# Performance work log

Hardware: AMD Instinct MI355X
Metric: run time of the kernel (lower is better)

The kernel has to match this reference:

```python
import jax, jax.numpy as jnp
import numpy as np

DIM_B = 4096   # batch of ragged segments
DIM_M = 128    # max seq len == dim_m == dim_c (source: dim_c = dim_m)
DIM_C = 128
DIM_Q = 256    # dim_q = 2 * dim_m


def _make_lengths():
    # deterministic ragged lengths in [1, DIM_M]; 37 coprime with 128 -> exact total
    return ((np.arange(DIM_B) * 37) % DIM_M + 1).astype(np.int64)


def setup_inputs() -> dict:
    key = jax.random.key(0)
    k1, k2, k3, k4 = jax.random.split(key, 4)
    xss = jax.random.normal(k1, (DIM_B, DIM_M, DIM_Q), dtype=jnp.float32)
    Wk = jax.random.normal(k2, (DIM_C, DIM_Q), dtype=jnp.float32) * 0.05
    Wc = jax.random.normal(k3, (DIM_M, DIM_C), dtype=jnp.float32) * 0.05
    proj = jax.random.normal(k4, (DIM_C, DIM_Q), dtype=jnp.float32) * 0.05
    lens = _make_lengths()
    # flat padded index (b*DIM_M + s) of every valid ragged token, in batch order
    gather_idx = np.concatenate([b * DIM_M + np.arange(l) for b, l in enumerate(lens)]).astype(np.int64)
    return {
        "xss": xss,
        "Wk": Wk,
        "Wc": Wc,
        "proj": proj,
        "seq_lengths": jnp.asarray(lens),
        "gather_idx": jnp.asarray(gather_idx),
    }


def reference(xss, Wk, Wc, proj, seq_lengths, gather_idx):
    B, M, Q = xss.shape
    # validity mask over padded positions
    mask = (jnp.arange(M)[None, :] < seq_lengths[:, None]).astype(xss.dtype)  # (B, M)
    # kernel: Linear(dim_q -> dim_c), applied to all (padded) tokens
    ks = jnp.einsum('bmq,cq->bmc', xss, Wk)          # (B, M, C)
    # pool: masked sum over the ragged segment
    context = jnp.einsum('bmc,bm->bc', ks, mask)     # (B, C)
    cs = context @ Wc.T                              # (B, C)  (dim_m == dim_c)
    v = cs @ proj                                    # (B, Q)
    y = jnp.einsum('bq,bmq->bm', v, xss)             # (B, M) per-token scalar
    # gather valid ragged tokens in original concat order -> (total_tokens, 1)
    ys = y.reshape(-1)[gather_idx][:, None]
    return ys
```

## Files before the change

kernel.cpp:

```cpp
#include <hip/hip_runtime.h>
#include <hip/hip_bf16.h>

#define DIM_B 4096
#define DIM_M 128
#define DIM_C 128
#define DIM_Q 256

__global__ __launch_bounds__(256) void k_xsum(const float* __restrict__ xss,
                                              const int* __restrict__ lens32,
                                              float* __restrict__ xsum) {
    const int b = blockIdx.x;
    const int tid = threadIdx.x;
    const int wave = tid >> 6, lane = tid & 63;
    const bool is64 = (lens32[1] == 0);
    const int len = is64 ? lens32[2 * b] : lens32[b];
    const float* base = xss + (size_t)b * DIM_M * DIM_Q + lane * 4;
    float a0 = 0.f, a1 = 0.f, a2 = 0.f, a3 = 0.f;
    for (int m = wave; m < len; m += 4) {
        const float4 u = *(const float4*)(base + (size_t)m * DIM_Q);
        a0 += u.x; a1 += u.y; a2 += u.z; a3 += u.w;
    }
    __shared__ float s[4][DIM_Q];
    s[wave][lane * 4 + 0] = a0;
    s[wave][lane * 4 + 1] = a1;
    s[wave][lane * 4 + 2] = a2;
    s[wave][lane * 4 + 3] = a3;
    __syncthreads();
    xsum[(size_t)b * DIM_Q + tid] = s[0][tid] + s[1][tid] + s[2][tid] + s[3][tid];
}

__global__ __launch_bounds__(256) void k_a1(const float* __restrict__ Wc,
                                            const float* __restrict__ proj,
                                            float* __restrict__ A1) {
    const int c = blockIdx.x;
    const int qp = threadIdx.x;
    float acc = 0.f;
    for (int j = 0; j < DIM_M; ++j)
        acc += Wc[j * DIM_C + c] * proj[j * DIM_Q + qp];
    A1[c * DIM_Q + qp] = acc;
}

__global__ __launch_bounds__(256) void k_wcomb(const float* __restrict__ Wk,
                                               const float* __restrict__ A1,
                                               float* __restrict__ Wcomb) {
    const int q = blockIdx.x;
    const int qp = threadIdx.x;
    float acc = 0.f;
    for (int c = 0; c < DIM_C; ++c)
        acc += Wk[c * DIM_Q + q] * A1[c * DIM_Q + qp];
    Wcomb[q * DIM_Q + qp] = acc;
}

__global__ __launch_bounds__(256) void k_v(const float* __restrict__ xsum,
                                           const float* __restrict__ Wcomb,
                                           float* __restrict__ v) {
    const int tid = threadIdx.x;
    const int b0 = blockIdx.x * 16;
    __shared__ float s[16][DIM_Q];
    for (int r = 0; r < 16; ++r)
        s[r][tid] = xsum[(size_t)(b0 + r) * DIM_Q + tid];
    __syncthreads();
    float acc[16];
#pragma unroll
    for (int r = 0; r < 16; ++r) acc[r] = 0.f;
    for (int q = 0; q < DIM_Q; ++q) {
        const float w = Wcomb[q * DIM_Q + tid];
#pragma unroll
        for (int r = 0; r < 16; ++r) acc[r] += s[r][q] * w;
    }
#pragma unroll
    for (int r = 0; r < 16; ++r)
        v[(size_t)(b0 + r) * DIM_Q + tid] = acc[r];
}

__global__ __launch_bounds__(256) void k_y(const float* __restrict__ xss,
                                           const float* __restrict__ v,
                                           const int* __restrict__ gidx32,
                                           float* __restrict__ out,
                                           int ntok) {
    const int wave = threadIdx.x >> 6, lane = threadIdx.x & 63;
    const int t = blockIdx.x * 4 + wave;
    if (t >= ntok) return;
    const bool is64 = (gidx32[1] == 0);
    const int idx = is64 ? gidx32[2 * t] : gidx32[t];
    const int b = idx >> 7;
    const float4 u  = *(const float4*)(xss + (size_t)idx * DIM_Q + lane * 4);
    const float4 vv = *(const float4*)(v + (size_t)b * DIM_Q + lane * 4);
    float d = u.x * vv.x + u.y * vv.y + u.z * vv.z + u.w * vv.w;
#pragma unroll
    for (int off = 32; off >= 1; off >>= 1)
        d += __shfl_down(d, off, 64);
    if (lane == 0)
        out[t] = d;
}

extern "C" void kernel_launch(void* const* d_in, const int* in_sizes, int n_in,
                              void* d_out, int out_size, void* d_ws, size_t ws_size,
                              hipStream_t stream) {
    const float* xss  = (const float*)d_in[0];
    const float* Wk   = (const float*)d_in[1];
    const float* Wc   = (const float*)d_in[2];
    const float* proj = (const float*)d_in[3];
    const int* lens = (const int*)d_in[4];
    const int* gidx = (const int*)d_in[5];
    float* out = (float*)d_out;
    const int ntok = in_sizes[5];

    float* ws    = (float*)d_ws;
    float* xsum  = ws;
    float* vbuf  = ws + (size_t)DIM_B * DIM_Q;
    float* A1    = vbuf + (size_t)DIM_B * DIM_Q;
    float* Wcomb = A1 + (size_t)DIM_C * DIM_Q;

    k_xsum<<<DIM_B, 256, 0, stream>>>(xss, lens, xsum);
    k_a1<<<DIM_C, 256, 0, stream>>>(Wc, proj, A1);
    k_wcomb<<<DIM_Q, 256, 0, stream>>>(Wk, A1, Wcomb);
    k_v<<<DIM_B / 16, 256, 0, stream>>>(xsum, Wcomb, vbuf);
    k_y<<<(ntok + 3) / 4, 256, 0, stream>>>(xss, vbuf, gidx, out, ntok);
}
```

Before: 744.4 us.

## Fuse pooling, projection and per-token dot into one kernel with LDS row staging

Replaces the xsum, v and y kernels with one per-batch kernel that sums the valid rows, computes v from Wcomb, and then computes per-token dot products. The first 56 rows are staged in shared memory so the second pass mostly avoids re-reading xss from HBM. Output offsets come from an in-block prefix sum of lengths instead of gather_idx. This trades heavy LDS use (lower occupancy) and redundant per-block Wcomb matvec and prefix-sum work for roughly halving global traffic.

```diff
diff --git a/kernel.cpp b/kernel.cpp
--- a/kernel.cpp
+++ b/kernel.cpp
@@ -1,33 +1,10 @@
 #include <hip/hip_runtime.h>
-#include <hip/hip_bf16.h>
 
 #define DIM_B 4096
 #define DIM_M 128
 #define DIM_C 128
 #define DIM_Q 256
-
-__global__ __launch_bounds__(256) void k_xsum(const float* __restrict__ xss,
-                                              const int* __restrict__ lens32,
-                                              float* __restrict__ xsum) {
-    const int b = blockIdx.x;
-    const int tid = threadIdx.x;
-    const int wave = tid >> 6, lane = tid & 63;
-    const bool is64 = (lens32[1] == 0);
-    const int len = is64 ? lens32[2 * b] : lens32[b];
-    const float* base = xss + (size_t)b * DIM_M * DIM_Q + lane * 4;
-    float a0 = 0.f, a1 = 0.f, a2 = 0.f, a3 = 0.f;
-    for (int m = wave; m < len; m += 4) {
-        const float4 u = *(const float4*)(base + (size_t)m * DIM_Q);
-        a0 += u.x; a1 += u.y; a2 += u.z; a3 += u.w;
-    }
-    __shared__ float s[4][DIM_Q];
-    s[wave][lane * 4 + 0] = a0;
-    s[wave][lane * 4 + 1] = a1;
-    s[wave][lane * 4 + 2] = a2;
-    s[wave][lane * 4 + 3] = a3;
-    __syncthreads();
-    xsum[(size_t)b * DIM_Q + tid] = s[0][tid] + s[1][tid] + s[2][tid] + s[3][tid];
-}
+#define NSTAGE 56
 
 __global__ __launch_bounds__(256) void k_a1(const float* __restrict__ Wc,
                                             const float* __restrict__ proj,
@@ -51,47 +28,75 @@
     Wcomb[q * DIM_Q + qp] = acc;
 }
 
-__global__ __launch_bounds__(256) void k_v(const float* __restrict__ xsum,
-                                           const float* __restrict__ Wcomb,
-                                           float* __restrict__ v) {
+__global__ __launch_bounds__(256) void k_fused(const float* __restrict__ xss,
+                                               const int* __restrict__ lens32,
+                                               const float* __restrict__ Wcomb,
+                                               float* __restrict__ out) {
+    const int b = blockIdx.x;
     const int tid = threadIdx.x;
-    const int b0 = blockIdx.x * 16;
-    __shared__ float s[16][DIM_Q];
-    for (int r = 0; r < 16; ++r)
-        s[r][tid] = xsum[(size_t)(b0 + r) * DIM_Q + tid];
+    const int wave = tid >> 6, lane = tid & 63;
+    const bool is64 = (lens32[1] == 0);
+
+    __shared__ float rows[NSTAGE * DIM_Q];
+    __shared__ float xsw[4][DIM_Q];
+    __shared__ float vv[DIM_Q];
+    __shared__ int wsum[4];
+    __shared__ int s_off;
+
+    const int len = is64 ? lens32[2 * b] : lens32[b];
+
+    int part = 0;
+    for (int i = tid; i < b; i += 256) part += is64 ? lens32[2 * i] : lens32[i];
+#pragma unroll
+    for (int off = 32; off >= 1; off >>= 1) part += __shfl_down(part, off, 64);
+    if (lane == 0) wsum[wave] = part;
     __syncthreads();
-    float acc[16];
+    if (tid == 0) s_off = wsum[0] + wsum[1] + wsum[2] + wsum[3];
+
+    const float* base = xss + (size_t)b * DIM_M * DIM_Q + lane * 4;
+    float a0 = 0.f, a1 = 0.f, a2 = 0.f, a3 = 0.f;
+    int m = wave;
+    for (; m + 4 < len; m += 8) {
+        const float4 u0 = *(const float4*)(base + (size_t)m * DIM_Q);
+        const float4 u1 = *(const float4*)(base + (size_t)(m + 4) * DIM_Q);
+        a0 += u0.x; a1 += u0.y; a2 += u0.z; a3 += u0.w;
+        a0 += u1.x; a1 += u1.y; a2 += u1.z; a3 += u1.w;
+        if (m < NSTAGE)     *(float4*)&rows[m * DIM_Q + lane * 4] = u0;
+        if (m + 4 < NSTAGE) *(float4*)&rows[(m + 4) * DIM_Q + lane * 4] = u1;
+    }
+    if (m < len) {
+        const float4 u0 = *(const float4*)(base + (size_t)m * DIM_Q);
+        a0 += u0.x; a1 += u0.y; a2 += u0.z; a3 += u0.w;
+        if (m < NSTAGE) *(float4*)&rows[m * DIM_Q + lane * 4] = u0;
+    }
+    xsw[wave][lane * 4 + 0] = a0;
+    xsw[wave][lane * 4 + 1] = a1;
+    xsw[wave][lane * 4 + 2] = a2;
+    xsw[wave][lane * 4 + 3] = a3;
+    __syncthreads();
+    xsw[0][tid] += xsw[1][tid] + xsw[2][tid] + xsw[3][tid];
+    __syncthreads();
+
+    {
+        float acc = 0.f;
+#pragma unroll 8
+        for (int q = 0; q < DIM_Q; ++q)
+            acc += xsw[0][q] * Wcomb[q * DIM_Q + tid];
+        vv[tid] = acc;
+    }
+    __syncthreads();
+
+    const float4 vreg = *(const float4*)&vv[lane * 4];
+    const int off0 = s_off;
+    for (int mm = wave; mm < len; mm += 4) {
+        const float4 x = (mm < NSTAGE)
+            ? *(const float4*)&rows[mm * DIM_Q + lane * 4]
+            : *(const float4*)(base + (size_t)mm * DIM_Q);
+        float d = x.x * vreg.x + x.y * vreg.y + x.z * vreg.z + x.w * vreg.w;
 #pragma unroll
-    for (int r = 0; r < 16; ++r) acc[r] = 0.f;
-    for (int q = 0; q < DIM_Q; ++q) {
-        const float w = Wcomb[q * DIM_Q + tid];
-#pragma unroll
-        for (int r = 0; r < 16; ++r) acc[r] += s[r][q] * w;
+        for (int off = 32; off >= 1; off >>= 1) d += __shfl_down(d, off, 64);
+        if (lane == 0) out[off0 + mm] = d;
     }
-#pragma unroll
-    for (int r = 0; r < 16; ++r)
-        v[(size_t)(b0 + r) * DIM_Q + tid] = acc[r];
-}
-
-__global__ __launch_bounds__(256) void k_y(const float* __restrict__ xss,
-                                           const float* __restrict__ v,
-                                           const int* __restrict__ gidx32,
-                                           float* __restrict__ out,
-                                           int ntok) {
-    const int wave = threadIdx.x >> 6, lane = threadIdx.x & 63;
-    const int t = blockIdx.x * 4 + wave;
-    if (t >= ntok) return;
-    const bool is64 = (gidx32[1] == 0);
-    const int idx = is64 ? gidx32[2 * t] : gidx32[t];
-    const int b = idx >> 7;
-    const float4 u  = *(const float4*)(xss + (size_t)idx * DIM_Q + lane * 4);
-    const float4 vv = *(const float4*)(v + (size_t)b * DIM_Q + lane * 4);
-    float d = u.x * vv.x + u.y * vv.y + u.z * vv.z + u.w * vv.w;
-#pragma unroll
-    for (int off = 32; off >= 1; off >>= 1)
-        d += __shfl_down(d, off, 64);
-    if (lane == 0)
-        out[t] = d;
 }
 
 extern "C" void kernel_launch(void* const* d_in, const int* in_sizes, int n_in,
@@ -102,19 +107,13 @@
     const float* Wc   = (const float*)d_in[2];
     const float* proj = (const float*)d_in[3];
     const int* lens = (const int*)d_in[4];
-    const int* gidx = (const int*)d_in[5];
     float* out = (float*)d_out;
-    const int ntok = in_sizes[5];
 
     float* ws    = (float*)d_ws;
-    float* xsum  = ws;
-    float* vbuf  = ws + (size_t)DIM_B * DIM_Q;
-    float* A1    = vbuf + (size_t)DIM_B * DIM_Q;
+    float* A1    = ws;
     float* Wcomb = A1 + (size_t)DIM_C * DIM_Q;
 
-    k_xsum<<<DIM_B, 256, 0, stream>>>(xss, lens, xsum);
     k_a1<<<DIM_C, 256, 0, stream>>>(Wc, proj, A1);
     k_wcomb<<<DIM_Q, 256, 0, stream>>>(Wk, A1, Wcomb);
-    k_v<<<DIM_B / 16, 256, 0, stream>>>(xsum, Wcomb, vbuf);
-    k_y<<<(ntok + 3) / 4, 256, 0, stream>>>(xss, vbuf, gidx, out, ntok);
+    k_fused<<<DIM_B, 256, 0, stream>>>(xss, lens, Wcomb, out);
 }
```

Result: no change. 754.8 us (+1.4%).
